# Performance work log

Measured on AMD Instinct MI355X. Metric: run time of the kernel, lower is better.

The kernel has to match this reference:

```python
import jax, jax.numpy as jnp
import numpy as np
import math

B, T, IN_DIM = 4, 1024, 64
D, H, L, DFF = 1024, 16, 4, 4096
N_STEPS = 24
MAXLEN = 2048
DK = D // H


def _pos_encoding(max_len, d):
    pos = np.arange(max_len, dtype=np.float32)[:, None]
    div = np.exp(np.arange(0, d, 2, dtype=np.float32) * (-math.log(10000.0) / d))
    pe = np.zeros((max_len, d), dtype=np.float32)
    pe[:, 0::2] = np.sin(pos * div)
    pe[:, 1::2] = np.cos(pos * div)
    return jnp.asarray(pe)

_PE = _pos_encoding(MAXLEN, D)


def _lin(x, W, b):
    # torch Linear convention: W is (out, in)
    return x @ W.T + b


def _mha(q, kv, Wq, bq, Wk, bk, Wv, bv, Wo, bo):
    Bq, Tq, _ = q.shape
    Tk = kv.shape[1]
    Qh = _lin(q, Wq, bq).reshape(Bq, Tq, H, DK).transpose(0, 2, 1, 3)
    Kh = _lin(kv, Wk, bk).reshape(Bq, Tk, H, DK).transpose(0, 2, 1, 3)
    Vh = _lin(kv, Wv, bv).reshape(Bq, Tk, H, DK).transpose(0, 2, 1, 3)
    scores = jnp.einsum('bhqd,bhkd->bhqk', Qh, Kh) / math.sqrt(DK)
    probs = jax.nn.softmax(scores, axis=-1)
    out = jnp.einsum('bhqk,bhkd->bhqd', probs, Vh)
    out = out.transpose(0, 2, 1, 3).reshape(Bq, Tq, D)
    return _lin(out, Wo, bo)


def _ffn(x, W1, b1, W2, b2):
    return _lin(jax.nn.relu(_lin(x, W1, b1)), W2, b2)


def _ln(x, g, b, eps=1e-5):
    mu = jnp.mean(x, axis=-1, keepdims=True)
    var = jnp.var(x, axis=-1, keepdims=True)
    return (x - mu) / jnp.sqrt(var + eps) * g + b


def setup_inputs() -> dict:
    key = jax.random.key(0)
    ks = iter(jax.random.split(key, 64))
    def w(shape, s=0.02):
        return jax.random.normal(next(ks), shape, jnp.float32) * s
    inp = {'x': jax.random.normal(next(ks), (B, T, IN_DIM), jnp.float32)}
    inp['in_W'] = w((D, IN_DIM)); inp['in_b'] = jnp.zeros((D,), jnp.float32)
    for p in ['enc', 'dec']:
        for n in ['Wq', 'Wk', 'Wv', 'Wo']:
            inp[f'{p}_{n}'] = w((L, D, D))
            inp[f'{p}_b{n[1].lower()}'] = jnp.zeros((L, D), jnp.float32)
    for p in ['ffe', 'ffd']:
        inp[f'{p}_W1'] = w((DFF, D)); inp[f'{p}_b1'] = jnp.zeros((DFF,), jnp.float32)
        inp[f'{p}_W2'] = w((D, DFF)); inp[f'{p}_b2'] = jnp.zeros((D,), jnp.float32)
    for p in ['ne', 'nd']:
        inp[f'{p}_g'] = jnp.ones((D,), jnp.float32); inp[f'{p}_b'] = jnp.zeros((D,), jnp.float32)
    inp['out_W'] = w((1, D)); inp['out_b'] = jnp.zeros((1,), jnp.float32)
    inp['temb_W'] = w((D, 1)); inp['temb_b'] = jnp.zeros((D,), jnp.float32)
    return inp


def reference(x, in_W, in_b,
              enc_Wq, enc_bq, enc_Wk, enc_bk, enc_Wv, enc_bv, enc_Wo, enc_bo,
              ffe_W1, ffe_b1, ffe_W2, ffe_b2, ne_g, ne_b,
              dec_Wq, dec_bq, dec_Wk, dec_bk, dec_Wv, dec_bv, dec_Wo, dec_bo,
              ffd_W1, ffd_b1, ffd_W2, ffd_b2, nd_g, nd_b,
              out_W, out_b, temb_W, temb_b):
    batch, seq, _ = x.shape
    h = _lin(x, in_W, in_b) + _PE[:seq]
    for l in range(L):
        h = _mha(h, h, enc_Wq[l], enc_bq[l], enc_Wk[l], enc_bk[l],
                 enc_Wv[l], enc_bv[l], enc_Wo[l], enc_bo[l])
        h = _ln(h + _ffn(h, ffe_W1, ffe_b1, ffe_W2, ffe_b2), ne_g, ne_b)
    dec = jnp.zeros((batch, 1, D), x.dtype)
    preds = []
    for _ in range(N_STEPS):
        d = dec + _PE[:dec.shape[1]]
        for l in range(L):
            # same layer weights used for self- and cross-attention, as in source
            d = _mha(d, d, dec_Wq[l], dec_bq[l], dec_Wk[l], dec_bk[l],
                     dec_Wv[l], dec_bv[l], dec_Wo[l], dec_bo[l])
            d = _mha(d, h, dec_Wq[l], dec_bq[l], dec_Wk[l], dec_bk[l],
                     dec_Wv[l], dec_bv[l], dec_Wo[l], dec_bo[l])
            d = _ln(d + _ffn(d, ffd_W1, ffd_b1, ffd_W2, ffd_b2), nd_g, nd_b)
        step = _lin(d[:, -1, :], out_W, out_b)        # (B, 1)
        preds.append(step[:, None, :])                 # (B, 1, 1)
        emb = _lin(step, temb_W, temb_b)[:, None, :]   # (B, 1, D)
        dec = jnp.concatenate([dec, emb], axis=1)
    return jnp.concatenate(preds, axis=1)              # (B, n_steps, 1)
```

## Files before the change

### kernel.cpp

```cpp
#include <hip/hip_runtime.h>
#include <math.h>

#define DM    1024
#define NH    16
#define DKH   64
#define NL    4
#define DFFN  4096
#define BB    4
#define TT    1024
#define NSTEP 24
#define BT    (BB*TT)
#define MD    (BB*NSTEP)
#define CSPLIT 8
#define CKEYS  (TT/CSPLIT)
#define PSTRIDE ((size_t)MD*DM)

typedef __attribute__((ext_vector_type(8))) short s16x8;
typedef __attribute__((ext_vector_type(4))) short s16x4;
typedef __attribute__((ext_vector_type(4))) float f32x4;

__device__ inline short f2b(float f){
  unsigned u = __float_as_uint(f);
  u += 0x7fffu + ((u>>16)&1u);
  return (short)(u>>16);
}
__device__ inline float b2f(short h){
  return __uint_as_float(((unsigned)(unsigned short)h)<<16);
}

__device__ inline float wave_sum(float v){
  #pragma unroll
  for (int off=1; off<64; off<<=1) v += __shfl_xor(v, off, 64);
  return v;
}

__global__ __launch_bounds__(256)
void split_kernel(const float* __restrict__ X, short* __restrict__ Hi,
                  short* __restrict__ Lo, int n8)
{
  const size_t i = (size_t)blockIdx.x*256 + threadIdx.x;
  if (i >= (size_t)n8) return;
  const float4 v0 = *(const float4*)(X + i*8);
  const float4 v1 = *(const float4*)(X + i*8 + 4);
  const float f[8] = {v0.x,v0.y,v0.z,v0.w,v1.x,v1.y,v1.z,v1.w};
  s16x8 hv, lv;
  #pragma unroll
  for (int e=0;e<8;e++){
    const short h = f2b(f[e]);
    hv[e] = h;
    lv[e] = f2b(f[e] - b2f(h));
  }
  *(s16x8*)(Hi + i*8) = hv;
  *(s16x8*)(Lo + i*8) = lv;
}

__global__ __launch_bounds__(256)
void split4_kernel(const float* __restrict__ X0, const float* __restrict__ X1,
                   const float* __restrict__ X2, const float* __restrict__ X3,
                   short* __restrict__ H0, short* __restrict__ L0,
                   short* __restrict__ H1, short* __restrict__ L1,
                   short* __restrict__ H2, short* __restrict__ L2,
                   short* __restrict__ H3, short* __restrict__ L3, int n8)
{
  const size_t i = (size_t)blockIdx.x*256 + threadIdx.x;
  if (i >= (size_t)n8) return;
  const int z = blockIdx.y;
  const float* X = (z==0)?X0:(z==1?X1:(z==2?X2:X3));
  short* Hi = (z==0)?H0:(z==1?H1:(z==2?H2:H3));
  short* Lo = (z==0)?L0:(z==1?L1:(z==2?L2:L3));
  const float4 v0 = *(const float4*)(X + i*8);
  const float4 v1 = *(const float4*)(X + i*8 + 4);
  const float f[8] = {v0.x,v0.y,v0.z,v0.w,v1.x,v1.y,v1.z,v1.w};
  s16x8 hv, lv;
  #pragma unroll
  for (int e=0;e<8;e++){
    const short h = f2b(f[e]);
    hv[e] = h;
    lv[e] = f2b(f[e] - b2f(h));
  }
  *(s16x8*)(Hi + i*8) = hv;
  *(s16x8*)(Lo + i*8) = lv;
}

__global__ __launch_bounds__(256)
void cvt_b(const float* __restrict__ X, short* __restrict__ O, int n8)
{
  const size_t i = (size_t)blockIdx.x*256 + threadIdx.x;
  if (i >= (size_t)n8) return;
  const float4 v0 = *(const float4*)(X + i*8);
  const float4 v1 = *(const float4*)(X + i*8 + 4);
  const float f[8] = {v0.x,v0.y,v0.z,v0.w,v1.x,v1.y,v1.z,v1.w};
  s16x8 hv;
  #pragma unroll
  for (int e=0;e<8;e++) hv[e] = f2b(f[e]);
  *(s16x8*)(O + i*8) = hv;
}

__global__ void zero_kernel(float* __restrict__ p, int n) {
  int i = blockIdx.x*256 + threadIdx.x;
  if (i < n) p[i] = 0.f;
}

__global__ __launch_bounds__(256)
void k_transpose(const float* __restrict__ A, float* __restrict__ At)
{
  __shared__ float tile[32][33];
  const int bx = blockIdx.x & 31, by = blockIdx.x >> 5;
  const int x0 = bx*32, y0 = by*32;
  const int tid = threadIdx.x;
  for (int i=tid; i<1024; i+=256){
    const int r = i>>5, c = i&31;
    tile[r][c] = A[(size_t)(y0+r)*DM + x0+c];
  }
  __syncthreads();
  for (int i=tid; i<1024; i+=256){
    const int r = i>>5, c = i&31;
    At[(size_t)(x0+r)*DM + y0+c] = tile[c][r];
  }
}

__global__ __launch_bounds__(256)
void k_bc(const float* __restrict__ Wq, const float* __restrict__ bo,
          const float* __restrict__ bq, float* __restrict__ bc)
{
  const int row = blockIdx.x, tid = threadIdx.x;
  float s = 0.f;
  for (int j=tid; j<DM; j+=256) s += Wq[(size_t)row*DM + j]*bo[j];
  s = wave_sum(s);
  __shared__ float r4[4];
  if ((tid&63)==0) r4[tid>>6] = s;
  __syncthreads();
  if (tid==0) bc[row] = r4[0]+r4[1]+r4[2]+r4[3] + bq[row];
}

__global__ __launch_bounds__(256)
void add_pe_split(const float* __restrict__ h, short* __restrict__ Hi,
                  short* __restrict__ Lo)
{
  const int row = blockIdx.x;
  const int pos = row & (TT-1);
  const int d = threadIdx.x*4;
  const float4 a = *(const float4*)(h + (size_t)row*DM + d);
  const float c1 = -9.210340371976184f / 1024.0f;
  const float e0 = expf((float)d * c1);
  const float e1 = expf((float)(d+2) * c1);
  const float a0 = (float)pos * e0, a1 = (float)pos * e1;
  const float v[4] = {a.x + sinf(a0), a.y + cosf(a0), a.z + sinf(a1), a.w + cosf(a1)};
  s16x4 hv, lv;
  #pragma unroll
  for (int e=0;e<4;e++){
    const short hb = f2b(v[e]);
    hv[e] = hb;
    lv[e] = f2b(v[e] - b2f(hb));
  }
  *(s16x4*)(Hi + (size_t)row*DM + d) = hv;
  *(s16x4*)(Lo + (size_t)row*DM + d) = lv;
}

template<int ACT, int OUT_MODE>
__global__ __launch_bounds__(256, 2)
void gemm_split(const short* __restrict__ Ahi, const short* __restrict__ Alo,
                const short* __restrict__ Bhi, const short* __restrict__ Blo,
                const float* __restrict__ bias,
                float* __restrict__ C, short* __restrict__ Chi, short* __restrict__ Clo,
                int M, int N, int K)
{
  __shared__ __align__(16) short lA[2][128][40];
  __shared__ __align__(16) short lB[2][128][40];
  const int tid = threadIdx.x;
  const int m0 = blockIdx.x*128, n0 = blockIdx.y*128;
  const int lane = tid & 63, w = tid >> 6;
  const int wr = w >> 1, wc = w & 1;
  const int fr = lane & 15, fq = lane >> 4;

  f32x4 acc[4][4];
  #pragma unroll
  for (int i=0;i<4;i++)
    #pragma unroll
    for (int j=0;j<4;j++) acc[i][j] = (f32x4){0.f,0.f,0.f,0.f};

  for (int k0 = 0; k0 < K; k0 += 32) {
    __syncthreads();
    #pragma unroll
    for (int j=0;j<2;j++){
      const int cc = tid + j*256;
      const int row = cc >> 2, kq = cc & 3;
      const size_t ga = (size_t)(m0+row)*K + k0 + kq*8;
      const size_t gb = (size_t)(n0+row)*K + k0 + kq*8;
      *(s16x8*)&lA[0][row][kq*8] = *(const s16x8*)(Ahi + ga);
      *(s16x8*)&lA[1][row][kq*8] = *(const s16x8*)(Alo + ga);
      *(s16x8*)&lB[0][row][kq*8] = *(const s16x8*)(Bhi + gb);
      *(s16x8*)&lB[1][row][kq*8] = *(const s16x8*)(Blo + gb);
    }
    __syncthreads();
    s16x8 ah[4], al[4], bh[4], bl[4];
    #pragma unroll
    for (int i=0;i<4;i++){
      ah[i] = *(const s16x8*)&lA[0][wr*64+i*16+fr][fq*8];
      al[i] = *(const s16x8*)&lA[1][wr*64+i*16+fr][fq*8];
    }
    #pragma unroll
    for (int j=0;j<4;j++){
      bh[j] = *(const s16x8*)&lB[0][wc*64+j*16+fr][fq*8];
      bl[j] = *(const s16x8*)&lB[1][wc*64+j*16+fr][fq*8];
    }
    #pragma unroll
    for (int i=0;i<4;i++)
      #pragma unroll
      for (int j=0;j<4;j++){
        acc[i][j] = __builtin_amdgcn_mfma_f32_16x16x32_bf16(ah[i], bh[j], acc[i][j], 0,0,0);
        acc[i][j] = __builtin_amdgcn_mfma_f32_16x16x32_bf16(ah[i], bl[j], acc[i][j], 0,0,0);
        acc[i][j] = __builtin_amdgcn_mfma_f32_16x16x32_bf16(al[i], bh[j], acc[i][j], 0,0,0);
      }
  }
  #pragma unroll
  for (int j=0;j<4;j++){
    const int col = n0 + wc*64 + j*16 + fr;
    const float bv = bias[col];
    #pragma unroll
    for (int i=0;i<4;i++){
      const int row0 = m0 + wr*64 + i*16 + fq*4;
      #pragma unroll
      for (int r=0;r<4;r++){
        float v = acc[i][j][r] + bv;
        if (ACT==1) v = fmaxf(v, 0.f);
        const size_t idx = (size_t)(row0+r)*N + col;
        if (OUT_MODE==0 || OUT_MODE==2) C[idx] = v;
        if (OUT_MODE==1 || OUT_MODE==2){
          const short hb = f2b(v);
          Chi[idx] = hb;
          Clo[idx] = f2b(v - b2f(hb));
        }
        if (OUT_MODE==3) Chi[idx] = f2b(v);
      }
    }
  }
}

__global__ __launch_bounds__(256, 2)
void gemm_split_qkv(const short* __restrict__ Ahi, const short* __restrict__ Alo,
                const short* __restrict__ B0h, const short* __restrict__ B0l,
                const short* __restrict__ B1h, const short* __restrict__ B1l,
                const short* __restrict__ B2h, const short* __restrict__ B2l,
                const float* __restrict__ b0, const float* __restrict__ b1,
                const float* __restrict__ b2,
                float* __restrict__ C0, float* __restrict__ C1, float* __restrict__ C2,
                int M, int N, int K)
{
  const int z = blockIdx.z;
  const short* Bhi = (z==0)?B0h:(z==1?B1h:B2h);
  const short* Blo = (z==0)?B0l:(z==1?B1l:B2l);
  const float* bias = (z==0)?b0:(z==1?b1:b2);
  float* C = (z==0)?C0:(z==1?C1:C2);
  __shared__ __align__(16) short lA[2][128][40];
  __shared__ __align__(16) short lB[2][128][40];
  const int tid = threadIdx.x;
  const int m0 = blockIdx.x*128, n0 = blockIdx.y*128;
  const int lane = tid & 63, w = tid >> 6;
  const int wr = w >> 1, wc = w & 1;
  const int fr = lane & 15, fq = lane >> 4;

  f32x4 acc[4][4];
  #pragma unroll
  for (int i=0;i<4;i++)
    #pragma unroll
    for (int j=0;j<4;j++) acc[i][j] = (f32x4){0.f,0.f,0.f,0.f};

  for (int k0 = 0; k0 < K; k0 += 32) {
    __syncthreads();
    #pragma unroll
    for (int j=0;j<2;j++){
      const int cc = tid + j*256;
      const int row = cc >> 2, kq = cc & 3;
      const size_t ga = (size_t)(m0+row)*K + k0 + kq*8;
      const size_t gb = (size_t)(n0+row)*K + k0 + kq*8;
      *(s16x8*)&lA[0][row][kq*8] = *(const s16x8*)(Ahi + ga);
      *(s16x8*)&lA[1][row][kq*8] = *(const s16x8*)(Alo + ga);
      *(s16x8*)&lB[0][row][kq*8] = *(const s16x8*)(Bhi + gb);
      *(s16x8*)&lB[1][row][kq*8] = *(const s16x8*)(Blo + gb);
    }
    __syncthreads();
    s16x8 ah[4], al[4], bh[4], bl[4];
    #pragma unroll
    for (int i=0;i<4;i++){
      ah[i] = *(const s16x8*)&lA[0][wr*64+i*16+fr][fq*8];
      al[i] = *(const s16x8*)&lA[1][wr*64+i*16+fr][fq*8];
    }
    #pragma unroll
    for (int j=0;j<4;j++){
      bh[j] = *(const s16x8*)&lB[0][wc*64+j*16+fr][fq*8];
      bl[j] = *(const s16x8*)&lB[1][wc*64+j*16+fr][fq*8];
    }
    #pragma unroll
    for (int i=0;i<4;i++)
      #pragma unroll
      for (int j=0;j<4;j++){
        acc[i][j] = __builtin_amdgcn_mfma_f32_16x16x32_bf16(ah[i], bh[j], acc[i][j], 0,0,0);
        acc[i][j] = __builtin_amdgcn_mfma_f32_16x16x32_bf16(ah[i], bl[j], acc[i][j], 0,0,0);
        acc[i][j] = __builtin_amdgcn_mfma_f32_16x16x32_bf16(al[i], bh[j], acc[i][j], 0,0,0);
      }
  }
  #pragma unroll
  for (int j=0;j<4;j++){
    const int col = n0 + wc*64 + j*16 + fr;
    const float bv = bias[col];
    #pragma unroll
    for (int i=0;i<4;i++){
      const int row0 = m0 + wr*64 + i*16 + fq*4;
      #pragma unroll
      for (int r=0;r<4;r++)
        C[(size_t)(row0+r)*N + col] = acc[i][j][r] + bv;
    }
  }
}

__global__ __launch_bounds__(256)
void attn_enc(const float* __restrict__ Qg, const float* __restrict__ Kg,
              const float* __restrict__ Vg, short* __restrict__ Ohi,
              short* __restrict__ Olo)
{
  const int bh = blockIdx.y;
  const int b = bh >> 4, hh = bh & 15;
  const int row = blockIdx.x*256 + threadIdx.x;
  const size_t base = ((size_t)b*TT)*DM + hh*DKH;
  float q[64];
  {
    const float* qp = Qg + base + (size_t)row*DM;
    #pragma unroll
    for (int d4=0; d4<16; d4++){
      const float4 v = *(const float4*)(qp + d4*4);
      q[d4*4+0]=v.x; q[d4*4+1]=v.y; q[d4*4+2]=v.z; q[d4*4+3]=v.w;
    }
  }
  float o[64];
  #pragma unroll
  for (int d=0;d<64;d++) o[d]=0.f;
  float m = -INFINITY, l = 0.f;
  __shared__ float Ks[64][68];
  __shared__ float Vs[64][68];
  for (int kt=0; kt<TT; kt+=64) {
    __syncthreads();
    #pragma unroll
    for (int t=0;t<4;t++){
      const int fi = threadIdx.x + t*256;
      const int j = fi>>4, dq = fi&15;
      *(float4*)&Ks[j][dq*4] = *(const float4*)(Kg + base + (size_t)(kt+j)*DM + dq*4);
      *(float4*)&Vs[j][dq*4] = *(const float4*)(Vg + base + (size_t)(kt+j)*DM + dq*4);
    }
    __syncthreads();
    for (int j=0;j<64;j++){
      float s0=0.f,s1=0.f,s2=0.f,s3=0.f;
      #pragma unroll
      for (int d=0; d<64; d+=4){
        s0 = fmaf(q[d+0], Ks[j][d+0], s0);
        s1 = fmaf(q[d+1], Ks[j][d+1], s1);
        s2 = fmaf(q[d+2], Ks[j][d+2], s2);
        s3 = fmaf(q[d+3], Ks[j][d+3], s3);
      }
      const float s = ((s0+s1)+(s2+s3)) * 0.125f;
      if (s > m) {
        const float f = __expf(m - s);
        l *= f;
        #pragma unroll
        for (int d=0;d<64;d++) o[d] *= f;
        m = s;
      }
      const float p = __expf(s - m);
      l += p;
      #pragma unroll
      for (int d=0;d<64;d++) o[d] = fmaf(p, Vs[j][d], o[d]);
    }
  }
  const float inv = 1.f / l;
  #pragma unroll
  for (int d8=0; d8<8; d8++){
    s16x8 hv, lv;
    #pragma unroll
    for (int e=0;e<8;e++){
      const float f = o[d8*8+e]*inv;
      const short hb = f2b(f);
      hv[e] = hb;
      lv[e] = f2b(f - b2f(hb));
    }
    *(s16x8*)(Ohi + base + (size_t)row*DM + d8*8) = hv;
    *(s16x8*)(Olo + base + (size_t)row*DM + d8*8) = lv;
  }
}

__global__ __launch_bounds__(256)
void ln_add_split(const float* __restrict__ X, const float* __restrict__ Y,
                  const float* __restrict__ g, const float* __restrict__ be,
                  short* __restrict__ Ohi, short* __restrict__ Olo)
{
  const size_t row = blockIdx.x;
  const int tid = threadIdx.x;
  const float4 a = *(const float4*)(X + row*DM + tid*4);
  const float4 b = *(const float4*)(Y + row*DM + tid*4);
  const float v0=a.x+b.x, v1=a.y+b.y, v2=a.z+b.z, v3=a.w+b.w;
  float s = v0+v1+v2+v3;
  float q = v0*v0+v1*v1+v2*v2+v3*v3;
  s = wave_sum(s); q = wave_sum(q);
  __shared__ float rs[4], rq[4];
  if ((tid&63)==0){ rs[tid>>6]=s; rq[tid>>6]=q; }
  __syncthreads();
  const float S = rs[0]+rs[1]+rs[2]+rs[3];
  const float Q = rq[0]+rq[1]+rq[2]+rq[3];
  const float mean = S * (1.f/DM);
  const float var  = Q * (1.f/DM) - mean*mean;
  const float rstd = rsqrtf(var + 1e-5f);
  const float4 gv = *(const float4*)(g  + tid*4);
  const float4 bv = *(const float4*)(be + tid*4);
  const float v[4] = {(v0-mean)*rstd*gv.x + bv.x, (v1-mean)*rstd*gv.y + bv.y,
                      (v2-mean)*rstd*gv.z + bv.z, (v3-mean)*rstd*gv.w + bv.w};
  s16x4 hv, lv;
  #pragma unroll
  for (int e=0;e<4;e++){
    const short hb = f2b(v[e]);
    hv[e] = hb;
    lv[e] = f2b(v[e] - b2f(hb));
  }
  *(s16x4*)(Ohi + row*DM + tid*4) = hv;
  *(s16x4*)(Olo + row*DM + tid*4) = lv;
}


template<int MR>
__global__ __launch_bounds__(256)
void gemm_dec(const short* __restrict__ Ahi, const short* __restrict__ Alo,
              const short* __restrict__ B0, const short* __restrict__ B1,
              const short* __restrict__ B2,
              float* __restrict__ part, int N, int K, int KS)
{
  const short* B = (blockIdx.z==0) ? B0 : (blockIdx.z==1 ? B1 : B2);
  float* P = part + ((size_t)blockIdx.z*KS + blockIdx.y)*(size_t)MD*N;
  const int KK = K / KS;
  const int kbase = blockIdx.y * KK;
  const int n0 = blockIdx.x * 128;
  __shared__ __align__(16) short lA[2][96][40];
  __shared__ __align__(16) short lB[128][40];
  const int tid = threadIdx.x;
  const int lane = tid & 63, w = tid >> 6;
  const int fr = lane & 15, fq = lane >> 4;
  constexpr int CH = MR*128;

  f32x4 acc[MR][2];
  #pragma unroll
  for (int i=0;i<MR;i++){ acc[i][0]=(f32x4){0,0,0,0}; acc[i][1]=(f32x4){0,0,0,0}; }

  for (int k0 = kbase; k0 < kbase + KK; k0 += 32) {
    __syncthreads();
    #pragma unroll
    for (int t=0; t<(CH+255)/256; t++){
      const int cc = tid + t*256;
      if (cc < CH){
        const int row = cc>>3, hl = (cc>>2)&1, kq = cc&3;
        const short* src = hl ? Alo : Ahi;
        *(s16x8*)&lA[hl][row][kq*8] = *(const s16x8*)(src + (size_t)row*K + k0 + kq*8);
      }
    }
    #pragma unroll
    for (int t=0; t<2; t++){
      const int cc = tid + t*256;
      const int row = cc>>2, kq = cc&3;
      *(s16x8*)&lB[row][kq*8] = *(const s16x8*)(B + (size_t)(n0+row)*K + k0 + kq*8);
    }
    __syncthreads();
    s16x8 bq[2];
    #pragma unroll
    for (int j=0;j<2;j++) bq[j] = *(const s16x8*)&lB[w*32+j*16+fr][fq*8];
    #pragma unroll
    for (int i=0;i<MR;i++){
      const s16x8 ah = *(const s16x8*)&lA[0][i*16+fr][fq*8];
      const s16x8 al = *(const s16x8*)&lA[1][i*16+fr][fq*8];
      #pragma unroll
      for (int j=0;j<2;j++){
        acc[i][j] = __builtin_amdgcn_mfma_f32_16x16x32_bf16(ah, bq[j], acc[i][j], 0,0,0);
        acc[i][j] = __builtin_amdgcn_mfma_f32_16x16x32_bf16(al, bq[j], acc[i][j], 0,0,0);
      }
    }
  }
  #pragma unroll
  for (int j=0;j<2;j++){
    const int col = n0 + w*32 + j*16 + fr;
    #pragma unroll
    for (int i=0;i<MR;i++){
      const int row0 = i*16 + fq*4;
      #pragma unroll
      for (int r=0;r<4;r++)
        P[(size_t)(row0+r)*N + col] = acc[i][j][r];
    }
  }
}

template<int MR, int AACT>
__global__ __launch_bounds__(256)
void gemm_dec_r(const float* __restrict__ PA, const float* __restrict__ biasA,
                const short* __restrict__ B,
                float* __restrict__ part, int N, int K, int KS)
{
  float* P = part + (size_t)blockIdx.y*(size_t)MD*N;
  const int KK = K / KS;
  const int kbase = blockIdx.y * KK;
  const int n0 = blockIdx.x * 128;
  __shared__ __align__(16) short lA[2][96][40];
  __shared__ __align__(16) short lB[128][40];
  const int tid = threadIdx.x;
  const int lane = tid & 63, w = tid >> 6;
  const int fr = lane & 15, fq = lane >> 4;
  constexpr int CH = MR*128;
  const size_t psA = (size_t)MD*K;

  f32x4 acc[MR][2];
  #pragma unroll
  for (int i=0;i<MR;i++){ acc[i][0]=(f32x4){0,0,0,0}; acc[i][1]=(f32x4){0,0,0,0}; }

  for (int k0 = kbase; k0 < kbase + KK; k0 += 32) {
    __syncthreads();
    #pragma unroll
    for (int t=0; t<(CH+255)/256; t++){
      const int cc = tid + t*256;
      if (cc < CH){
        const int row = cc>>3, q = cc&7;
        const int k = k0 + q*4;
        float4 a = *(const float4*)(biasA + k);
        const float* src = PA + (size_t)row*K + k;
        #pragma unroll
        for (int p=0;p<8;p++){
          const float4 v = *(const float4*)(src + (size_t)p*psA);
          a.x+=v.x; a.y+=v.y; a.z+=v.z; a.w+=v.w;
        }
        if (AACT){
          a.x=fmaxf(a.x,0.f); a.y=fmaxf(a.y,0.f);
          a.z=fmaxf(a.z,0.f); a.w=fmaxf(a.w,0.f);
        }
        const float vv[4] = {a.x,a.y,a.z,a.w};
        s16x4 hv, lv;
        #pragma unroll
        for (int e=0;e<4;e++){
          const short hb = f2b(vv[e]);
          hv[e] = hb;
          lv[e] = f2b(vv[e] - b2f(hb));
        }
        *(s16x4*)&lA[0][row][q*4] = hv;
        *(s16x4*)&lA[1][row][q*4] = lv;
      }
    }
    #pragma unroll
    for (int t=0; t<2; t++){
      const int cc = tid + t*256;
      const int row = cc>>2, kq = cc&3;
      *(s16x8*)&lB[row][kq*8] = *(const s16x8*)(B + (size_t)(n0+row)*K + k0 + kq*8);
    }
    __syncthreads();
    s16x8 bq[2];
    #pragma unroll
    for (int j=0;j<2;j++) bq[j] = *(const s16x8*)&lB[w*32+j*16+fr][fq*8];
    #pragma unroll
    for (int i=0;i<MR;i++){
      const s16x8 ah = *(const s16x8*)&lA[0][i*16+fr][fq*8];
      const s16x8 al = *(const s16x8*)&lA[1][i*16+fr][fq*8];
      #pragma unroll
      for (int j=0;j<2;j++){
        acc[i][j] = __builtin_amdgcn_mfma_f32_16x16x32_bf16(ah, bq[j], acc[i][j], 0,0,0);
        acc[i][j] = __builtin_amdgcn_mfma_f32_16x16x32_bf16(al, bq[j], acc[i][j], 0,0,0);
      }
    }
  }
  #pragma unroll
  for (int j=0;j<2;j++){
    const int col = n0 + w*32 + j*16 + fr;
    #pragma unroll
    for (int i=0;i<MR;i++){
      const int row0 = i*16 + fq*4;
      #pragma unroll
      for (int r=0;r<4;r++)
        P[(size_t)(row0+r)*N + col] = acc[i][j][r];
    }
  }
}

template<int MR>
__global__ __launch_bounds__(256)
void gemm_dec_c(const float* __restrict__ opart, const float* __restrict__ mlp,
                const short* __restrict__ B,
                float* __restrict__ part, int N, int K, int KS, int n)
{
  float* P = part + (size_t)blockIdx.y*(size_t)MD*N;
  const int KK = K / KS;
  const int kbase = blockIdx.y * KK;
  const int n0 = blockIdx.x * 128;
  __shared__ __align__(16) short lA[2][96][40];
  __shared__ __align__(16) short lB[128][40];
  const int tid = threadIdx.x;
  const int lane = tid & 63, w = tid >> 6;
  const int fr = lane & 15, fq = lane >> 4;
  constexpr int CH = MR*128;

  f32x4 acc[MR][2];
  #pragma unroll
  for (int i=0;i<MR;i++){ acc[i][0]=(f32x4){0,0,0,0}; acc[i][1]=(f32x4){0,0,0,0}; }

  for (int k0 = kbase; k0 < kbase + KK; k0 += 32) {
    __syncthreads();
    const int hh = k0 >> 6;
    #pragma unroll
    for (int t=0; t<(CH+255)/256; t++){
      const int cc = tid + t*256;
      if (cc < CH){
        const int row = cc>>3, q = cc&7;
        const int d = (k0 & 63) + q*4;
        const int b = row & 3, i = row >> 2;
        const int bh = b*16 + hh;
        float4 a = {0.f,0.f,0.f,0.f};
        if (i < n){
          const float* ml = mlp + (size_t)bh*CSPLIT*(2*NSTEP) + i*2;
          float M = -INFINITY;
          #pragma unroll
          for (int s=0;s<CSPLIT;s++)
            M = fmaxf(M, ml[(size_t)s*(2*NSTEP)]);
          float L = 0.f;
          #pragma unroll
          for (int s=0;s<CSPLIT;s++){
            const float mm = ml[(size_t)s*(2*NSTEP)];
            const float ll = ml[(size_t)s*(2*NSTEP) + 1];
            const float f = __expf(mm - M);
            const float4 v = *(const float4*)(opart +
                (((size_t)(bh*CSPLIT+s)*NSTEP + i)*DKH + d));
            a.x = fmaf(f, v.x, a.x); a.y = fmaf(f, v.y, a.y);
            a.z = fmaf(f, v.z, a.z); a.w = fmaf(f, v.w, a.w);
            L = fmaf(f, ll, L);
          }
          const float inv = 1.f / L;
          a.x*=inv; a.y*=inv; a.z*=inv; a.w*=inv;
        }
        const float vv[4] = {a.x,a.y,a.z,a.w};
        s16x4 hv, lv;
        #pragma unroll
        for (int e=0;e<4;e++){
          const short hb = f2b(vv[e]);
          hv[e] = hb;
          lv[e] = f2b(vv[e] - b2f(hb));
        }
        *(s16x4*)&lA[0][row][q*4] = hv;
        *(s16x4*)&lA[1][row][q*4] = lv;
      }
    }
    #pragma unroll
    for (int t=0; t<2; t++){
      const int cc = tid + t*256;
      const int row = cc>>2, kq = cc&3;
      *(s16x8*)&lB[row][kq*8] = *(const s16x8*)(B + (size_t)(n0+row)*K + k0 + kq*8);
    }
    __syncthreads();
    s16x8 bq[2];
    #pragma unroll
    for (int j=0;j<2;j++) bq[j] = *(const s16x8*)&lB[w*32+j*16+fr][fq*8];
    #pragma unroll
    for (int i=0;i<MR;i++){
      const s16x8 ah = *(const s16x8*)&lA[0][i*16+fr][fq*8];
      const s16x8 al = *(const s16x8*)&lA[1][i*16+fr][fq*8];
      #pragma unroll
      for (int j=0;j<2;j++){
        acc[i][j] = __builtin_amdgcn_mfma_f32_16x16x32_bf16(ah, bq[j], acc[i][j], 0,0,0);
        acc[i][j] = __builtin_amdgcn_mfma_f32_16x16x32_bf16(al, bq[j], acc[i][j], 0,0,0);
      }
    }
  }
  #pragma unroll
  for (int j=0;j<2;j++){
    const int col = n0 + w*32 + j*16 + fr;
    #pragma unroll
    for (int i=0;i<MR;i++){
      const int row0 = i*16 + fq*4;
      #pragma unroll
      for (int r=0;r<4;r++)
        P[(size_t)(row0+r)*N + col] = acc[i][j][r];
    }
  }
}

__global__ __launch_bounds__(256)
void attn_qkv(const float* __restrict__ part,
              const float* __restrict__ lbq, const float* __restrict__ lbk,
              const float* __restrict__ lbv,
              short* __restrict__ Ohi, short* __restrict__ Olo, int n)
{
  const int bh = blockIdx.x, b = bh >> 4, hh = bh & 15;
  const size_t obase = (size_t)b*DM + hh*DKH;
  __shared__ float Qs[NSTEP][68], Ks[NSTEP][68], Vs[NSTEP][68];
  __shared__ float P[NSTEP][28];
  const int tid = threadIdx.x;
  for (int t = tid; t < 3*n*16; t += 256){
    const int tensor = t / (n*16);
    const int fi = t - tensor*(n*16);
    const int row = fi >> 4, q4 = fi & 15;
    const int col0 = hh*DKH + q4*4;
    const float* bias = (tensor==0?lbq:(tensor==1?lbk:lbv));
    float4 a;
    a.x = bias[col0]; a.y = bias[col0+1]; a.z = bias[col0+2]; a.w = bias[col0+3];
    const size_t eoff = (size_t)(row*4+b)*DM + col0;
    #pragma unroll
    for (int ks=0; ks<8; ks++){
      const float4 p = *(const float4*)(part + (size_t)(tensor*8+ks)*PSTRIDE + eoff);
      a.x+=p.x; a.y+=p.y; a.z+=p.z; a.w+=p.w;
    }
    float (*dst)[68] = (tensor==0?Qs:(tensor==1?Ks:Vs));
    *(float4*)&dst[row][q4*4] = a;
  }
  __syncthreads();
  for (int idx = tid; idx < n*n; idx += 256){
    const int i = idx / n, j = idx - i*n;
    float s0=0.f,s1=0.f,s2=0.f,s3=0.f;
    #pragma unroll
    for (int d=0; d<64; d+=4){
      s0 = fmaf(Qs[i][d+0], Ks[j][d+0], s0);
      s1 = fmaf(Qs[i][d+1], Ks[j][d+1], s1);
      s2 = fmaf(Qs[i][d+2], Ks[j][d+2], s2);
      s3 = fmaf(Qs[i][d+3], Ks[j][d+3], s3);
    }
    P[i][j] = ((s0+s1)+(s2+s3))*0.125f;
  }
  __syncthreads();
  if (tid < n){
    float mm = -INFINITY;
    for (int j=0;j<n;j++) mm = fmaxf(mm, P[tid][j]);
    float l = 0.f;
    for (int j=0;j<n;j++){ const float p = __expf(P[tid][j]-mm); P[tid][j]=p; l+=p; }
    const float inv = 1.f/l;
    for (int j=0;j<n;j++) P[tid][j] *= inv;
  }
  __syncthreads();
  for (int idx = tid; idx < n*64; idx += 256){
    const int i = idx >> 6, d = idx & 63;
    float s = 0.f;
    for (int j=0;j<n;j++) s = fmaf(P[i][j], Vs[j][d], s);
    const short hb = f2b(s);
    const size_t o = obase + (size_t)(i*4)*DM + d;
    Ohi[o] = hb;
    Olo[o] = f2b(s - b2f(hb));
  }
}

__global__ __launch_bounds__(256)
void attn_cross_part(const float* __restrict__ Qpart, const float* __restrict__ lbc,
                     const short* __restrict__ Kc, const short* __restrict__ Vc,
                     float* __restrict__ opart, float* __restrict__ mlpart, int n)
{
  const int ks = blockIdx.x, bh = blockIdx.y;
  const int b = bh >> 4, hh = bh & 15;
  __shared__ float Qs[NSTEP][68];
  __shared__ short KVs[CKEYS][72];
  __shared__ float S[NSTEP][132];
  const int tid = threadIdx.x;
  for (int t=tid; t<n*16; t+=256){
    const int row = t>>4, q4 = t&15;
    const int col0 = hh*DKH + q4*4;
    float4 a;
    a.x = lbc[col0]; a.y = lbc[col0+1]; a.z = lbc[col0+2]; a.w = lbc[col0+3];
    const size_t eoff = (size_t)(row*4+b)*DM + col0;
    #pragma unroll
    for (int p=0; p<8; p++){
      const float4 v = *(const float4*)(Qpart + (size_t)p*PSTRIDE + eoff);
      a.x+=v.x; a.y+=v.y; a.z+=v.z; a.w+=v.w;
    }
    *(float4*)&Qs[row][q4*4] = a;
  }
  const size_t kbase = ((size_t)b*TT + (size_t)ks*CKEYS)*DM + hh*DKH;
  for (int t=tid; t<CKEYS*8; t+=256){
    const int row = t>>3, d8 = t&7;
    *(s16x8*)&KVs[row][d8*8] = *(const s16x8*)(Kc + kbase + (size_t)row*DM + d8*8);
  }
  __syncthreads();
  for (int idx=tid; idx<n*128; idx+=256){
    const int i = idx >> 7, j = idx & 127;
    float s0=0.f,s1=0.f,s2=0.f,s3=0.f;
    #pragma unroll
    for (int d=0; d<64; d+=4){
      s0 = fmaf(Qs[i][d+0], b2f(KVs[j][d+0]), s0);
      s1 = fmaf(Qs[i][d+1], b2f(KVs[j][d+1]), s1);
      s2 = fmaf(Qs[i][d+2], b2f(KVs[j][d+2]), s2);
      s3 = fmaf(Qs[i][d+3], b2f(KVs[j][d+3]), s3);
// ... 365 lines not shown
```

Baseline: 13.33 ms.

## Prefetch next K-tile into registers in split-bf16 GEMM kernels

The GEMM main loops of gemm_split, gemm_split_qkv and gemm_dec now issue global loads for the next K-slice into registers before running the MFMAs on the current LDS tile, then write them to LDS after a barrier. This is meant to hide global memory latency behind the matrix math instead of stalling at each tile load. Launch bounds drop the min-2-blocks hint so the compiler has room for the extra staging registers, at the risk of lower occupancy.

```diff
diff --git a/kernel.cpp b/kernel.cpp
--- a/kernel.cpp
+++ b/kernel.cpp
@@ -158,7 +158,7 @@
 }
 
 template<int ACT, int OUT_MODE>
-__global__ __launch_bounds__(256, 2)
+__global__ __launch_bounds__(256)
 void gemm_split(const short* __restrict__ Ahi, const short* __restrict__ Alo,
                 const short* __restrict__ Bhi, const short* __restrict__ Blo,
                 const float* __restrict__ bias,
@@ -173,26 +173,48 @@
   const int wr = w >> 1, wc = w & 1;
   const int fr = lane & 15, fq = lane >> 4;
 
+  int srow[2], skq[2];
+  #pragma unroll
+  for (int j=0;j<2;j++){ const int cc = tid + j*256; srow[j]=cc>>2; skq[j]=cc&3; }
+  s16x8 rAh[2], rAl[2], rBh[2], rBl[2];
+
   f32x4 acc[4][4];
   #pragma unroll
   for (int i=0;i<4;i++)
     #pragma unroll
     for (int j=0;j<4;j++) acc[i][j] = (f32x4){0.f,0.f,0.f,0.f};
 
+  #pragma unroll
+  for (int j=0;j<2;j++){
+    const size_t ga = (size_t)(m0+srow[j])*K + skq[j]*8;
+    const size_t gb = (size_t)(n0+srow[j])*K + skq[j]*8;
+    rAh[j] = *(const s16x8*)(Ahi + ga);
+    rAl[j] = *(const s16x8*)(Alo + ga);
+    rBh[j] = *(const s16x8*)(Bhi + gb);
+    rBl[j] = *(const s16x8*)(Blo + gb);
+  }
+  #pragma unroll
+  for (int j=0;j<2;j++){
+    *(s16x8*)&lA[0][srow[j]][skq[j]*8] = rAh[j];
+    *(s16x8*)&lA[1][srow[j]][skq[j]*8] = rAl[j];
+    *(s16x8*)&lB[0][srow[j]][skq[j]*8] = rBh[j];
+    *(s16x8*)&lB[1][srow[j]][skq[j]*8] = rBl[j];
+  }
+  __syncthreads();
+
   for (int k0 = 0; k0 < K; k0 += 32) {
-    __syncthreads();
-    #pragma unroll
-    for (int j=0;j<2;j++){
-      const int cc = tid + j*256;
-      const int row = cc >> 2, kq = cc & 3;
-      const size_t ga = (size_t)(m0+row)*K + k0 + kq*8;
-      const size_t gb = (size_t)(n0+row)*K + k0 + kq*8;
-      *(s16x8*)&lA[0][row][kq*8] = *(const s16x8*)(Ahi + ga);
-      *(s16x8*)&lA[1][row][kq*8] = *(const s16x8*)(Alo + ga);
-      *(s16x8*)&lB[0][row][kq*8] = *(const s16x8*)(Bhi + gb);
-      *(s16x8*)&lB[1][row][kq*8] = *(const s16x8*)(Blo + gb);
-    }
-    __syncthreads();
+    const int kn = k0 + 32;
+    if (kn < K){
+      #pragma unroll
+      for (int j=0;j<2;j++){
+        const size_t ga = (size_t)(m0+srow[j])*K + kn + skq[j]*8;
+        const size_t gb = (size_t)(n0+srow[j])*K + kn + skq[j]*8;
+        rAh[j] = *(const s16x8*)(Ahi + ga);
+        rAl[j] = *(const s16x8*)(Alo + ga);
+        rBh[j] = *(const s16x8*)(Bhi + gb);
+        rBl[j] = *(const s16x8*)(Blo + gb);
+      }
+    }
     s16x8 ah[4], al[4], bh[4], bl[4];
     #pragma unroll
     for (int i=0;i<4;i++){
@@ -212,6 +234,17 @@
         acc[i][j] = __builtin_amdgcn_mfma_f32_16x16x32_bf16(ah[i], bl[j], acc[i][j], 0,0,0);
         acc[i][j] = __builtin_amdgcn_mfma_f32_16x16x32_bf16(al[i], bh[j], acc[i][j], 0,0,0);
       }
+    __syncthreads();
+    if (kn < K){
+      #pragma unroll
+      for (int j=0;j<2;j++){
+        *(s16x8*)&lA[0][srow[j]][skq[j]*8] = rAh[j];
+        *(s16x8*)&lA[1][srow[j]][skq[j]*8] = rAl[j];
+        *(s16x8*)&lB[0][srow[j]][skq[j]*8] = rBh[j];
+        *(s16x8*)&lB[1][srow[j]][skq[j]*8] = rBl[j];
+      }
+      __syncthreads();
+    }
   }
   #pragma unroll
   for (int j=0;j<4;j++){
@@ -237,7 +270,7 @@
   }
 }
 
-__global__ __launch_bounds__(256, 2)
+__global__ __launch_bounds__(256)
 void gemm_split_qkv(const short* __restrict__ Ahi, const short* __restrict__ Alo,
                 const short* __restrict__ B0h, const short* __restrict__ B0l,
                 const short* __restrict__ B1h, const short* __restrict__ B1l,
@@ -260,26 +293,48 @@
   const int wr = w >> 1, wc = w & 1;
   const int fr = lane & 15, fq = lane >> 4;
 
+  int srow[2], skq[2];
+  #pragma unroll
+  for (int j=0;j<2;j++){ const int cc = tid + j*256; srow[j]=cc>>2; skq[j]=cc&3; }
+  s16x8 rAh[2], rAl[2], rBh[2], rBl[2];
+
   f32x4 acc[4][4];
   #pragma unroll
   for (int i=0;i<4;i++)
     #pragma unroll
     for (int j=0;j<4;j++) acc[i][j] = (f32x4){0.f,0.f,0.f,0.f};
 
+  #pragma unroll
+  for (int j=0;j<2;j++){
+    const size_t ga = (size_t)(m0+srow[j])*K + skq[j]*8;
+    const size_t gb = (size_t)(n0+srow[j])*K + skq[j]*8;
+    rAh[j] = *(const s16x8*)(Ahi + ga);
+    rAl[j] = *(const s16x8*)(Alo + ga);
+    rBh[j] = *(const s16x8*)(Bhi + gb);
+    rBl[j] = *(const s16x8*)(Blo + gb);
+  }
+  #pragma unroll
+  for (int j=0;j<2;j++){
+    *(s16x8*)&lA[0][srow[j]][skq[j]*8] = rAh[j];
+    *(s16x8*)&lA[1][srow[j]][skq[j]*8] = rAl[j];
+    *(s16x8*)&lB[0][srow[j]][skq[j]*8] = rBh[j];
+    *(s16x8*)&lB[1][srow[j]][skq[j]*8] = rBl[j];
+  }
+  __syncthreads();
+
   for (int k0 = 0; k0 < K; k0 += 32) {
-    __syncthreads();
-    #pragma unroll
-    for (int j=0;j<2;j++){
-      const int cc = tid + j*256;
-      const int row = cc >> 2, kq = cc & 3;
-      const size_t ga = (size_t)(m0+row)*K + k0 + kq*8;
-      const size_t gb = (size_t)(n0+row)*K + k0 + kq*8;
-      *(s16x8*)&lA[0][row][kq*8] = *(const s16x8*)(Ahi + ga);
-      *(s16x8*)&lA[1][row][kq*8] = *(const s16x8*)(Alo + ga);
-      *(s16x8*)&lB[0][row][kq*8] = *(const s16x8*)(Bhi + gb);
-      *(s16x8*)&lB[1][row][kq*8] = *(const s16x8*)(Blo + gb);
-    }
-    __syncthreads();
+    const int kn = k0 + 32;
+    if (kn < K){
+      #pragma unroll
+      for (int j=0;j<2;j++){
+        const size_t ga = (size_t)(m0+srow[j])*K + kn + skq[j]*8;
+        const size_t gb = (size_t)(n0+srow[j])*K + kn + skq[j]*8;
+        rAh[j] = *(const s16x8*)(Ahi + ga);
+        rAl[j] = *(const s16x8*)(Alo + ga);
+        rBh[j] = *(const s16x8*)(Bhi + gb);
+        rBl[j] = *(const s16x8*)(Blo + gb);
+      }
+    }
     s16x8 ah[4], al[4], bh[4], bl[4];
     #pragma unroll
     for (int i=0;i<4;i++){
@@ -299,6 +354,17 @@
         acc[i][j] = __builtin_amdgcn_mfma_f32_16x16x32_bf16(ah[i], bl[j], acc[i][j], 0,0,0);
         acc[i][j] = __builtin_amdgcn_mfma_f32_16x16x32_bf16(al[i], bh[j], acc[i][j], 0,0,0);
       }
+    __syncthreads();
+    if (kn < K){
+      #pragma unroll
+      for (int j=0;j<2;j++){
+        *(s16x8*)&lA[0][srow[j]][skq[j]*8] = rAh[j];
+        *(s16x8*)&lA[1][srow[j]][skq[j]*8] = rAl[j];
+        *(s16x8*)&lB[0][srow[j]][skq[j]*8] = rBh[j];
+        *(s16x8*)&lB[1][srow[j]][skq[j]*8] = rBl[j];
+      }
+      __syncthreads();
+    }
   }
   #pragma unroll
   for (int j=0;j<4;j++){
@@ -442,29 +508,51 @@
   const int lane = tid & 63, w = tid >> 6;
   const int fr = lane & 15, fq = lane >> 4;
   constexpr int CH = MR*128;
+  constexpr int NT = (CH+255)/256;
+
+  int arow[NT], akq[NT]; const short* asrc[NT]; bool aval[NT];
+  #pragma unroll
+  for (int t=0;t<NT;t++){
+    const int cc = tid + t*256;
+    aval[t] = cc < CH;
+    arow[t] = cc>>3; akq[t] = cc&3;
+    asrc[t] = ((cc>>2)&1) ? Alo : Ahi;
+  }
+  int brow[2], bkq[2];
+  #pragma unroll
+  for (int t=0;t<2;t++){ const int cc = tid + t*256; brow[t]=cc>>2; bkq[t]=cc&3; }
+  s16x8 ra[NT], rb[2];
 
   f32x4 acc[MR][2];
   #pragma unroll
   for (int i=0;i<MR;i++){ acc[i][0]=(f32x4){0,0,0,0}; acc[i][1]=(f32x4){0,0,0,0}; }
 
+  #pragma unroll
+  for (int t=0;t<NT;t++) if (aval[t])
+    ra[t] = *(const s16x8*)(asrc[t] + (size_t)arow[t]*K + kbase + akq[t]*8);
+  #pragma unroll
+  for (int t=0;t<2;t++)
+    rb[t] = *(const s16x8*)(B + (size_t)(n0+brow[t])*K + kbase + bkq[t]*8);
+  #pragma unroll
+  for (int t=0;t<NT;t++) if (aval[t]){
+    short* dst = ((tid + t*256)>>2)&1 ? &lA[1][arow[t]][akq[t]*8] : &lA[0][arow[t]][akq[t]*8];
+    *(s16x8*)dst = ra[t];
+  }
+  #pragma unroll
+  for (int t=0;t<2;t++) *(s16x8*)&lB[brow[t]][bkq[t]*8] = rb[t];
+  __syncthreads();
+
   for (int k0 = kbase; k0 < kbase + KK; k0 += 32) {
-    __syncthreads();
-    #pragma unroll
-    for (int t=0; t<(CH+255)/256; t++){
-      const int cc = tid + t*256;
-      if (cc < CH){
-        const int row = cc>>3, hl = (cc>>2)&1, kq = cc&3;
-        const short* src = hl ? Alo : Ahi;
-        *(s16x8*)&lA[hl][row][kq*8] = *(const s16x8*)(src + (size_t)row*K + k0 + kq*8);
-      }
-    }
-    #pragma unroll
-    for (int t=0; t<2; t++){
-      const int cc = tid + t*256;
-      const int row = cc>>2, kq = cc&3;
-      *(s16x8*)&lB[row][kq*8] = *(const s16x8*)(B + (size_t)(n0+row)*K + k0 + kq*8);
-    }
-    __syncthreads();
+    const int kn = k0 + 32;
+    const bool more = kn < kbase + KK;
+    if (more){
+      #pragma unroll
+      for (int t=0;t<NT;t++) if (aval[t])
+        ra[t] = *(const s16x8*)(asrc[t] + (size_t)arow[t]*K + kn + akq[t]*8);
+      #pragma unroll
+      for (int t=0;t<2;t++)
+        rb[t] = *(const s16x8*)(B + (size_t)(n0+brow[t])*K + kn + bkq[t]*8);
+    }
     s16x8 bq[2];
     #pragma unroll
     for (int j=0;j<2;j++) bq[j] = *(const s16x8*)&lB[w*32+j*16+fr][fq*8];
@@ -477,6 +565,17 @@
         acc[i][j] = __builtin_amdgcn_mfma_f32_16x16x32_bf16(ah, bq[j], acc[i][j], 0,0,0);
         acc[i][j] = __builtin_amdgcn_mfma_f32_16x16x32_bf16(al, bq[j], acc[i][j], 0,0,0);
       }
+    }
+    __syncthreads();
+    if (more){
+      #pragma unroll
+      for (int t=0;t<NT;t++) if (aval[t]){
+        short* dst = ((tid + t*256)>>2)&1 ? &lA[1][arow[t]][akq[t]*8] : &lA[0][arow[t]][akq[t]*8];
+        *(s16x8*)dst = ra[t];
+      }
+      #pragma unroll
+      for (int t=0;t<2;t++) *(s16x8*)&lB[brow[t]][bkq[t]*8] = rb[t];
+      __syncthreads();
     }
   }
   #pragma unroll
```

Result: no change. 13.36 ms (+0.2%).
